# Optimization experiments

Measured on AMD Instinct MI355X. Metric: run time of the kernel, lower is better.

Reference implementation:

```python
import jax, jax.numpy as jnp
import numpy as np

INPUT_DIM, HIDDEN_DIM, OUTPUT_DIM = 64, 512, 64
BATCH, SEQ = 256, 512


def setup_inputs() -> dict:
    key = jax.random.key(0)
    ks = jax.random.split(key, 7)
    s_x = 1.0 / np.sqrt(INPUT_DIM)
    s_h = 1.0 / np.sqrt(HIDDEN_DIM)
    return {
        "x": jax.random.normal(ks[0], (BATCH, SEQ, INPUT_DIM), dtype=jnp.float32),
        "Wx": jax.random.uniform(ks[1], (HIDDEN_DIM, INPUT_DIM), minval=-s_x, maxval=s_x, dtype=jnp.float32),
        "bx": jax.random.uniform(ks[2], (HIDDEN_DIM,), minval=-s_x, maxval=s_x, dtype=jnp.float32),
        "Wh": jax.random.uniform(ks[3], (HIDDEN_DIM, HIDDEN_DIM), minval=-s_h, maxval=s_h, dtype=jnp.float32),
        "bh": jax.random.uniform(ks[4], (HIDDEN_DIM,), minval=-s_h, maxval=s_h, dtype=jnp.float32),
        "Wy": jax.random.uniform(ks[5], (OUTPUT_DIM, HIDDEN_DIM), minval=-s_h, maxval=s_h, dtype=jnp.float32),
        "by": jax.random.uniform(ks[6], (OUTPUT_DIM,), minval=-s_h, maxval=s_h, dtype=jnp.float32),
    }


def reference(x, Wx, bx, Wh, bh, Wy, by):
    # x: [B, T, I]. Precompute the input projection for all steps (one big GEMM),
    # then scan the sequential recurrence h_t = tanh(xproj_t + h_{t-1} @ Wh^T + bh).
    B = x.shape[0]
    xproj = jnp.einsum('bti,hi->bth', x, Wx) + bx  # [B, T, H]
    h0 = jnp.zeros((B, Wh.shape[0]), dtype=x.dtype)

    def step(h, xp_t):
        h = jnp.tanh(xp_t + h @ Wh.T + bh)
        return h, None

    hT, _ = jax.lax.scan(step, h0, jnp.swapaxes(xproj, 0, 1))  # scan over T
    y = hT @ Wy.T + by  # [B, O]
    return y
```

## Files before the change

### kernel.cpp

```cpp
#include <hip/hip_runtime.h>
#include <hip/hip_fp16.h>
#include <cstdint>
#include <cstddef>


constexpr int BATCH = 256;
constexpr int SEQ   = 512;
constexpr int IN    = 64;
constexpr int HID   = 512;
constexpr int OUT   = 64;
constexpr int T     = 512;
constexpr int DTOT  = HID + IN;
constexpr int DSL   = DTOT / 8;
constexpr int NL    = 19;
constexpr int KL0   = 53;

typedef _Float16 half2v __attribute__((ext_vector_type(2)));

__device__ __forceinline__ float fdot2(uint32_t w, uint32_t h, float acc) {
    return __builtin_amdgcn_fdot2(__builtin_bit_cast(half2v, w),
                                  __builtin_bit_cast(half2v, h), acc, false);
}
__device__ __forceinline__ uint32_t packh2(float lo, float hi) {
    return (uint32_t)__half_as_ushort(__float2half(lo)) |
           ((uint32_t)__half_as_ushort(__float2half(hi)) << 16);
}
template <int CTRL>
__device__ __forceinline__ float dpp_add(float v) {
    int i = __builtin_bit_cast(int, v);
    int p = __builtin_amdgcn_update_dpp(i, i, CTRL, 0xF, 0xF, false);
    return v + __builtin_bit_cast(float, p);
}

__global__ __launch_bounds__(256, 1)
void prep_w(const float* __restrict__ Wh, const float* __restrict__ Wx,
            uint4* __restrict__ Wpk) {
    const int idx = blockIdx.x * 256 + threadIdx.x;
    const int k = idx >> 9, t = idx & (T - 1);
    const int p = k >> 3, r = k & 7;
    const int g = t >> 3, s = t & 7;
    const int o = 8 * g + r;
    const int d0 = DSL * s + 8 * p;
    const float* src = (d0 < HID) ? (Wh + (size_t)o * HID + d0)
                                  : (Wx + (size_t)o * IN + (d0 - HID));
    uint4 d;
    d.x = packh2(src[0], src[1]);
    d.y = packh2(src[2], src[3]);
    d.z = packh2(src[4], src[5]);
    d.w = packh2(src[6], src[7]);
    Wpk[idx] = d;
}

#define MV(f, Z) { \
    Z = fdot2(w##f.x, hv.x, Z); Z = fdot2(w##f.y, hv.y, Z); \
    Z = fdot2(w##f.z, hv.z, Z); Z = fdot2(w##f.w, hv.w, Z); }
#define ML(i, Z) { const uint4 wv = wl[t * NL + (i)]; \
    Z = fdot2(wv.x, hv.x, Z); Z = fdot2(wv.y, hv.y, Z); \
    Z = fdot2(wv.z, hv.z, Z); Z = fdot2(wv.w, hv.w, Z); }

__global__ __launch_bounds__(T, 2)
__attribute__((amdgpu_waves_per_eu(2, 2)))
void rnn_main(const float* __restrict__ x,  const float* __restrict__ bx,
              const float* __restrict__ bh, const float* __restrict__ Wy,
              const float* __restrict__ by, const uint4* __restrict__ Wpk,
              float* __restrict__ y) {
    __shared__ uint4 wl[T * NL];
    __shared__ __align__(16) __half hb2[2][DTOT];

    const int b = blockIdx.x, t = threadIdx.x;
    const int s = t & 7;

    {
        uint32_t agk;
        asm volatile("v_accvgpr_write_b32 a127, 0\n\t"
                     "s_nop 1\n\t"
                     "v_accvgpr_read_b32 %0, a127" : "=v"(agk));
        if (agk == 0xDEADBEEFu) hb2[0][0] = __float2half(0.0f);
    }

    #pragma unroll
    for (int i = 0; i < NL; ++i)
        wl[t * NL + i] = Wpk[(size_t)(KL0 + i) * T + t];

#define DECL_WV(f) const uint4 w##f = Wpk[(size_t)(f) * T + t];
    DECL_WV(0)  DECL_WV(1)  DECL_WV(2)  DECL_WV(3)  DECL_WV(4)  DECL_WV(5)
    DECL_WV(6)  DECL_WV(7)  DECL_WV(8)  DECL_WV(9)  DECL_WV(10) DECL_WV(11)
    DECL_WV(12) DECL_WV(13) DECL_WV(14) DECL_WV(15) DECL_WV(16) DECL_WV(17)
    DECL_WV(18) DECL_WV(19) DECL_WV(20) DECL_WV(21) DECL_WV(22) DECL_WV(23)
    DECL_WV(24) DECL_WV(25) DECL_WV(26) DECL_WV(27) DECL_WV(28) DECL_WV(29)
    DECL_WV(30) DECL_WV(31) DECL_WV(32) DECL_WV(33) DECL_WV(34) DECL_WV(35)
    DECL_WV(36) DECL_WV(37) DECL_WV(38) DECL_WV(39) DECL_WV(40) DECL_WV(41)
    DECL_WV(42) DECL_WV(43) DECL_WV(44) DECL_WV(45) DECL_WV(46) DECL_WV(47)
    DECL_WV(48) DECL_WV(49) DECL_WV(50) DECL_WV(51) DECL_WV(52)
#undef DECL_WV

    const float bs = bx[t] + bh[t];
    const float* xb = x + (size_t)b * SEQ * IN;

    hb2[0][t] = __float2half(0.0f);
    if (t < IN) hb2[0][HID + t] = __float2half(xb[t]);
    float xv = (t < IN) ? xb[IN + t] : 0.0f;
    __syncthreads();

    #pragma unroll 1
    for (int tt = 0; tt < SEQ; ++tt) {
        const int c = tt & 1;
        const uint4* hb = (const uint4*)(&hb2[c][0] + DSL * s);
        float z0 = 0.f, z1 = 0.f, z2 = 0.f, z3 = 0.f;
        float z4 = 0.f, z5 = 0.f, z6 = 0.f, z7 = 0.f;

        { const uint4 hv = hb[0];
          MV(0,z0) MV(1,z1) MV(2,z2) MV(3,z3) MV(4,z4) MV(5,z5) MV(6,z6) MV(7,z7) }
        { const uint4 hv = hb[1];
          MV(8,z0) MV(9,z1) MV(10,z2) MV(11,z3) MV(12,z4) MV(13,z5) MV(14,z6) MV(15,z7) }
        { const uint4 hv = hb[2];
          MV(16,z0) MV(17,z1) MV(18,z2) MV(19,z3) MV(20,z4) MV(21,z5) MV(22,z6) MV(23,z7) }
        { const uint4 hv = hb[3];
          MV(24,z0) MV(25,z1) MV(26,z2) MV(27,z3) MV(28,z4) MV(29,z5) MV(30,z6) MV(31,z7) }
        { const uint4 hv = hb[4];
          MV(32,z0) MV(33,z1) MV(34,z2) MV(35,z3) MV(36,z4) MV(37,z5) MV(38,z6) MV(39,z7) }
        { const uint4 hv = hb[5];
          MV(40,z0) MV(41,z1) MV(42,z2) MV(43,z3) MV(44,z4) MV(45,z5) MV(46,z6) MV(47,z7) }
        { const uint4 hv = hb[6];
          MV(48,z0) MV(49,z1) MV(50,z2) MV(51,z3) MV(52,z4) ML(0,z5) ML(1,z6) ML(2,z7) }
        { const uint4 hv = hb[7];
          ML(3,z0) ML(4,z1) ML(5,z2) ML(6,z3) ML(7,z4) ML(8,z5) ML(9,z6) ML(10,z7) }
        { const uint4 hv = hb[8];
          ML(11,z0) ML(12,z1) ML(13,z2) ML(14,z3) ML(15,z4) ML(16,z5) ML(17,z6) ML(18,z7) }

        z0 = dpp_add<0xB1>(z0); z0 = dpp_add<0x4E>(z0); z0 = dpp_add<0x141>(z0);
        z1 = dpp_add<0xB1>(z1); z1 = dpp_add<0x4E>(z1); z1 = dpp_add<0x141>(z1);
        z2 = dpp_add<0xB1>(z2); z2 = dpp_add<0x4E>(z2); z2 = dpp_add<0x141>(z2);
        z3 = dpp_add<0xB1>(z3); z3 = dpp_add<0x4E>(z3); z3 = dpp_add<0x141>(z3);
        z4 = dpp_add<0xB1>(z4); z4 = dpp_add<0x4E>(z4); z4 = dpp_add<0x141>(z4);
        z5 = dpp_add<0xB1>(z5); z5 = dpp_add<0x4E>(z5); z5 = dpp_add<0x141>(z5);
        z6 = dpp_add<0xB1>(z6); z6 = dpp_add<0x4E>(z6); z6 = dpp_add<0x141>(z6);
        z7 = dpp_add<0xB1>(z7); z7 = dpp_add<0x4E>(z7); z7 = dpp_add<0x141>(z7);

        const float za = (s & 1) ? z1 : z0;
        const float zb = (s & 1) ? z3 : z2;
        const float zc = (s & 1) ? z5 : z4;
        const float zd = (s & 1) ? z7 : z6;
        const float ze = (s & 2) ? zb : za;
        const float zf = (s & 2) ? zd : zc;
        const float zz = (s & 4) ? zf : ze;
        const float hh = 1.f - 2.f * __builtin_amdgcn_rcpf(__expf(2.f * (zz + bs)) + 1.f);
        hb2[c ^ 1][t] = __float2half(hh);

        if (t < IN) {
            hb2[c ^ 1][HID + t] = __float2half(xv);
            if (tt + 2 < SEQ) xv = xb[(size_t)(tt + 2) * IN + t];
        }
        __syncthreads();
    }

    if (t < OUT) {
        float acc = by[t];
        const float* wy = Wy + (size_t)t * HID;
        #pragma unroll 8
        for (int j = 0; j < HID; ++j)
            acc = fmaf(wy[j], __half2float(hb2[0][j]), acc);
        y[(size_t)b * OUT + t] = acc;
    }
}

extern "C" void kernel_launch(void* const* d_in, const int* in_sizes, int n_in,
                              void* d_out, int out_size, void* d_ws, size_t ws_size,
                              hipStream_t stream) {
    const float* x  = (const float*)d_in[0];
    const float* Wx = (const float*)d_in[1];
    const float* bx = (const float*)d_in[2];
    const float* Wh = (const float*)d_in[3];
    const float* bh = (const float*)d_in[4];
    const float* Wy = (const float*)d_in[5];
    const float* by = (const float*)d_in[6];
    float* y = (float*)d_out;

    uint4* Wpk = (uint4*)d_ws;

    hipLaunchKernelGGL(prep_w, dim3(72 * T / 256), dim3(256), 0, stream,
                       Wh, Wx, Wpk);
    hipLaunchKernelGGL(rnn_main, dim3(BATCH), dim3(T), 0, stream,
                       x, bx, bh, Wy, by, Wpk, y);
}
```

Before: 879.2 us.

## Precompute input projection in separate GEMM kernel and shrink recurrent matvec

Adds a prep_xp kernel that computes x@Wx^T+bx for every batch and step into an fp16 workspace buffer. The recurrent kernel then only does the 512x512 hidden matvec (64 packed weight slices instead of 72) and adds the prefetched projection per step. This removes the x columns from the serial loop and reduces LDS-resident weights, at the cost of writing and reading a 128 MB fp16 intermediate and an extra launch. Falls back to the old path if the workspace is too small.

```diff
diff --git a/kernel.cpp b/kernel.cpp
--- a/kernel.cpp
+++ b/kernel.cpp
@@ -10,10 +10,6 @@
 constexpr int HID   = 512;
 constexpr int OUT   = 64;
 constexpr int T     = 512;
-constexpr int DTOT  = HID + IN;
-constexpr int DSL   = DTOT / 8;
-constexpr int NL    = 19;
-constexpr int KL0   = 53;
 
 typedef _Float16 half2v __attribute__((ext_vector_type(2)));
 
@@ -32,17 +28,14 @@
     return v + __builtin_bit_cast(float, p);
 }
 
+
 __global__ __launch_bounds__(256, 1)
-void prep_w(const float* __restrict__ Wh, const float* __restrict__ Wx,
-            uint4* __restrict__ Wpk) {
+void prep_w64(const float* __restrict__ Wh, uint4* __restrict__ Wpk) {
     const int idx = blockIdx.x * 256 + threadIdx.x;
     const int k = idx >> 9, t = idx & (T - 1);
     const int p = k >> 3, r = k & 7;
     const int g = t >> 3, s = t & 7;
-    const int o = 8 * g + r;
-    const int d0 = DSL * s + 8 * p;
-    const float* src = (d0 < HID) ? (Wh + (size_t)o * HID + d0)
-                                  : (Wx + (size_t)o * IN + (d0 - HID));
+    const float* src = Wh + (size_t)(8 * g + r) * HID + (64 * s + 8 * p);
     uint4 d;
     d.x = packh2(src[0], src[1]);
     d.y = packh2(src[2], src[3]);
@@ -51,21 +44,56 @@
     Wpk[idx] = d;
 }
 
+__global__ __launch_bounds__(256, 1)
+void prep_xp(const float* __restrict__ x, const float* __restrict__ Wx,
+             const float* __restrict__ bx, __half* __restrict__ XPh) {
+    __shared__ uint32_t xs2[16][32];
+    const int tid = threadIdx.x;
+    const size_t R0 = (size_t)blockIdx.x * 16;
+
+    for (int e = tid; e < 16 * 32; e += 256) {
+        const int r = e >> 5, j = e & 31;
+        const float2 v = *(const float2*)(x + (R0 + r) * IN + 2 * j);
+        xs2[r][j] = packh2(v.x, v.y);
+    }
+    const int c0 = 2 * tid, c1 = c0 + 1;
+    uint32_t wa[32], wb[32];
+    #pragma unroll
+    for (int q = 0; q < 16; ++q) {
+        const float4 va = *(const float4*)(Wx + (size_t)c0 * IN + 4 * q);
+        wa[2 * q] = packh2(va.x, va.y); wa[2 * q + 1] = packh2(va.z, va.w);
+        const float4 vb = *(const float4*)(Wx + (size_t)c1 * IN + 4 * q);
+        wb[2 * q] = packh2(vb.x, vb.y); wb[2 * q + 1] = packh2(vb.z, vb.w);
+    }
+    const float b0 = bx[c0], b1 = bx[c1];
+    __syncthreads();
+
+    for (int r = 0; r < 16; ++r) {
+        float a0 = b0, a1 = b1;
+        #pragma unroll
+        for (int j = 0; j < 32; ++j) {
+            const uint32_t hx = xs2[r][j];
+            a0 = fdot2(wa[j], hx, a0);
+            a1 = fdot2(wb[j], hx, a1);
+        }
+        ((uint32_t*)XPh)[((R0 + r) * HID + c0) >> 1] = packh2(a0, a1);
+    }
+}
+
 #define MV(f, Z) { \
     Z = fdot2(w##f.x, hv.x, Z); Z = fdot2(w##f.y, hv.y, Z); \
     Z = fdot2(w##f.z, hv.z, Z); Z = fdot2(w##f.w, hv.w, Z); }
-#define ML(i, Z) { const uint4 wv = wl[t * NL + (i)]; \
+#define ML(i, Z) { const uint4 wv = wl[(i) * T + t]; \
     Z = fdot2(wv.x, hv.x, Z); Z = fdot2(wv.y, hv.y, Z); \
     Z = fdot2(wv.z, hv.z, Z); Z = fdot2(wv.w, hv.w, Z); }
 
 __global__ __launch_bounds__(T, 2)
 __attribute__((amdgpu_waves_per_eu(2, 2)))
-void rnn_main(const float* __restrict__ x,  const float* __restrict__ bx,
-              const float* __restrict__ bh, const float* __restrict__ Wy,
-              const float* __restrict__ by, const uint4* __restrict__ Wpk,
-              float* __restrict__ y) {
-    __shared__ uint4 wl[T * NL];
-    __shared__ __align__(16) __half hb2[2][DTOT];
+void rnn_main64(const float* __restrict__ bh, const float* __restrict__ Wy,
+                const float* __restrict__ by, const uint4* __restrict__ Wpk,
+                const __half* __restrict__ XPh, float* __restrict__ y) {
+    __shared__ uint4 wl[11 * T];
+    __shared__ __align__(16) __half hb2[2][HID];
 
     const int b = blockIdx.x, t = threadIdx.x;
     const int s = t & 7;
@@ -79,8 +107,8 @@
     }
 
     #pragma unroll
-    for (int i = 0; i < NL; ++i)
-        wl[t * NL + i] = Wpk[(size_t)(KL0 + i) * T + t];
+    for (int i = 0; i < 11; ++i)
+        wl[i * T + t] = Wpk[(size_t)(53 + i) * T + t];
 
 #define DECL_WV(f) const uint4 w##f = Wpk[(size_t)(f) * T + t];
     DECL_WV(0)  DECL_WV(1)  DECL_WV(2)  DECL_WV(3)  DECL_WV(4)  DECL_WV(5)
@@ -94,18 +122,20 @@
     DECL_WV(48) DECL_WV(49) DECL_WV(50) DECL_WV(51) DECL_WV(52)
 #undef DECL_WV
 
-    const float bs = bx[t] + bh[t];
-    const float* xb = x + (size_t)b * SEQ * IN;
+    const float bs = bh[t];
+    const __half* XProw = XPh + ((size_t)b * SEQ) * HID + t;
 
     hb2[0][t] = __float2half(0.0f);
-    if (t < IN) hb2[0][HID + t] = __float2half(xb[t]);
-    float xv = (t < IN) ? xb[IN + t] : 0.0f;
+    float xpc = __half2float(XProw[0]);
     __syncthreads();
 
     #pragma unroll 1
     for (int tt = 0; tt < SEQ; ++tt) {
         const int c = tt & 1;
-        const uint4* hb = (const uint4*)(&hb2[c][0] + DSL * s);
+        float xpn = 0.0f;
+        if (tt + 1 < SEQ) xpn = __half2float(XProw[(size_t)(tt + 1) * HID]);
+
+        const uint4* hb = (const uint4*)(&hb2[c][0] + 64 * s);
         float z0 = 0.f, z1 = 0.f, z2 = 0.f, z3 = 0.f;
         float z4 = 0.f, z5 = 0.f, z6 = 0.f, z7 = 0.f;
 
@@ -125,8 +155,136 @@
           MV(48,z0) MV(49,z1) MV(50,z2) MV(51,z3) MV(52,z4) ML(0,z5) ML(1,z6) ML(2,z7) }
         { const uint4 hv = hb[7];
           ML(3,z0) ML(4,z1) ML(5,z2) ML(6,z3) ML(7,z4) ML(8,z5) ML(9,z6) ML(10,z7) }
+
+        z0 = dpp_add<0xB1>(z0); z0 = dpp_add<0x4E>(z0); z0 = dpp_add<0x141>(z0);
+        z1 = dpp_add<0xB1>(z1); z1 = dpp_add<0x4E>(z1); z1 = dpp_add<0x141>(z1);
+        z2 = dpp_add<0xB1>(z2); z2 = dpp_add<0x4E>(z2); z2 = dpp_add<0x141>(z2);
+        z3 = dpp_add<0xB1>(z3); z3 = dpp_add<0x4E>(z3); z3 = dpp_add<0x141>(z3);
+        z4 = dpp_add<0xB1>(z4); z4 = dpp_add<0x4E>(z4); z4 = dpp_add<0x141>(z4);
+        z5 = dpp_add<0xB1>(z5); z5 = dpp_add<0x4E>(z5); z5 = dpp_add<0x141>(z5);
+        z6 = dpp_add<0xB1>(z6); z6 = dpp_add<0x4E>(z6); z6 = dpp_add<0x141>(z6);
+        z7 = dpp_add<0xB1>(z7); z7 = dpp_add<0x4E>(z7); z7 = dpp_add<0x141>(z7);
+
+        const float za = (s & 1) ? z1 : z0;
+        const float zb = (s & 1) ? z3 : z2;
+        const float zc = (s & 1) ? z5 : z4;
+        const float zd = (s & 1) ? z7 : z6;
+        const float ze = (s & 2) ? zb : za;
+        const float zf = (s & 2) ? zd : zc;
+        const float zz = (s & 4) ? zf : ze;
+        const float hh = 1.f - 2.f * __builtin_amdgcn_rcpf(
+                             __expf(2.f * (zz + bs + xpc)) + 1.f);
+        hb2[c ^ 1][t] = __float2half(hh);
+        xpc = xpn;
+        __syncthreads();
+    }
+
+    if (t < OUT) {
+        float acc = by[t];
+        const float* wy = Wy + (size_t)t * HID;
+        #pragma unroll 8
+        for (int j = 0; j < HID; ++j)
+            acc = fmaf(wy[j], __half2float(hb2[0][j]), acc);
+        y[(size_t)b * OUT + t] = acc;
+    }
+}
+
+
+constexpr int DTOT  = HID + IN;
+constexpr int DSL72 = DTOT / 8;
+constexpr int NL72  = 19;
+constexpr int KL072 = 53;
+
+__global__ __launch_bounds__(256, 1)
+void prep_w72(const float* __restrict__ Wh, const float* __restrict__ Wx,
+              uint4* __restrict__ Wpk) {
+    const int idx = blockIdx.x * 256 + threadIdx.x;
+    const int k = idx >> 9, t = idx & (T - 1);
+    const int p = k >> 3, r = k & 7;
+    const int g = t >> 3, s = t & 7;
+    const int o = 8 * g + r;
+    const int d0 = DSL72 * s + 8 * p;
+    const float* src = (d0 < HID) ? (Wh + (size_t)o * HID + d0)
+                                  : (Wx + (size_t)o * IN + (d0 - HID));
+    uint4 d;
+    d.x = packh2(src[0], src[1]);
+    d.y = packh2(src[2], src[3]);
+    d.z = packh2(src[4], src[5]);
+    d.w = packh2(src[6], src[7]);
+    Wpk[idx] = d;
+}
+
+#define ML72(i, Z) { const uint4 wv = wl[t * NL72 + (i)]; \
+    Z = fdot2(wv.x, hv.x, Z); Z = fdot2(wv.y, hv.y, Z); \
+    Z = fdot2(wv.z, hv.z, Z); Z = fdot2(wv.w, hv.w, Z); }
+
+__global__ __launch_bounds__(T, 2)
+__attribute__((amdgpu_waves_per_eu(2, 2)))
+void rnn_main72(const float* __restrict__ x,  const float* __restrict__ bx,
+                const float* __restrict__ bh, const float* __restrict__ Wy,
+                const float* __restrict__ by, const uint4* __restrict__ Wpk,
+                float* __restrict__ y) {
+    __shared__ uint4 wl[T * NL72];
+    __shared__ __align__(16) __half hb2[2][DTOT];
+
+    const int b = blockIdx.x, t = threadIdx.x;
+    const int s = t & 7;
+    {
+        uint32_t agk;
+        asm volatile("v_accvgpr_write_b32 a127, 0\n\t"
+                     "s_nop 1\n\t"
+                     "v_accvgpr_read_b32 %0, a127" : "=v"(agk));
+        if (agk == 0xDEADBEEFu) hb2[0][0] = __float2half(0.0f);
+    }
+    #pragma unroll
+    for (int i = 0; i < NL72; ++i)
+        wl[t * NL72 + i] = Wpk[(size_t)(KL072 + i) * T + t];
+
+#define DECL_WV(f) const uint4 w##f = Wpk[(size_t)(f) * T + t];
+    DECL_WV(0)  DECL_WV(1)  DECL_WV(2)  DECL_WV(3)  DECL_WV(4)  DECL_WV(5)
+    DECL_WV(6)  DECL_WV(7)  DECL_WV(8)  DECL_WV(9)  DECL_WV(10) DECL_WV(11)
+    DECL_WV(12) DECL_WV(13) DECL_WV(14) DECL_WV(15) DECL_WV(16) DECL_WV(17)
+    DECL_WV(18) DECL_WV(19) DECL_WV(20) DECL_WV(21) DECL_WV(22) DECL_WV(23)
+    DECL_WV(24) DECL_WV(25) DECL_WV(26) DECL_WV(27) DECL_WV(28) DECL_WV(29)
+    DECL_WV(30) DECL_WV(31) DECL_WV(32) DECL_WV(33) DECL_WV(34) DECL_WV(35)
+    DECL_WV(36) DECL_WV(37) DECL_WV(38) DECL_WV(39) DECL_WV(40) DECL_WV(41)
+    DECL_WV(42) DECL_WV(43) DECL_WV(44) DECL_WV(45) DECL_WV(46) DECL_WV(47)
+    DECL_WV(48) DECL_WV(49) DECL_WV(50) DECL_WV(51) DECL_WV(52)
+#undef DECL_WV
+
+    const float bs = bx[t] + bh[t];
+    const float* xb = x + (size_t)b * SEQ * IN;
+
+    hb2[0][t] = __float2half(0.0f);
+    if (t < IN) hb2[0][HID + t] = __float2half(xb[t]);
+    float xv = (t < IN) ? xb[IN + t] : 0.0f;
+    __syncthreads();
+
+    #pragma unroll 1
+    for (int tt = 0; tt < SEQ; ++tt) {
+        const int c = tt & 1;
+        const uint4* hb = (const uint4*)(&hb2[c][0] + DSL72 * s);
+        float z0 = 0.f, z1 = 0.f, z2 = 0.f, z3 = 0.f;
+        float z4 = 0.f, z5 = 0.f, z6 = 0.f, z7 = 0.f;
+
+        { const uint4 hv = hb[0];
+          MV(0,z0) MV(1,z1) MV(2,z2) MV(3,z3) MV(4,z4) MV(5,z5) MV(6,z6) MV(7,z7) }
+        { const uint4 hv = hb[1];
+          MV(8,z0) MV(9,z1) MV(10,z2) MV(11,z3) MV(12,z4) MV(13,z5) MV(14,z6) MV(15,z7) }
+        { const uint4 hv = hb[2];
+          MV(16,z0) MV(17,z1) MV(18,z2) MV(19,z3) MV(20,z4) MV(21,z5) MV(22,z6) MV(23,z7) }
+        { const uint4 hv = hb[3];
+          MV(24,z0) MV(25,z1) MV(26,z2) MV(27,z3) MV(28,z4) MV(29,z5) MV(30,z6) MV(31,z7) }
+        { const uint4 hv = hb[4];
+          MV(32,z0) MV(33,z1) MV(34,z2) MV(35,z3) MV(36,z4) MV(37,z5) MV(38,z6) MV(39,z7) }
+        { const uint4 hv = hb[5];
+          MV(40,z0) MV(41,z1) MV(42,z2) MV(43,z3) MV(44,z4) MV(45,z5) MV(46,z6) MV(47,z7) }
+        { const uint4 hv = hb[6];
+          MV(48,z0) MV(49,z1) MV(50,z2) MV(51,z3) MV(52,z4) ML72(0,z5) ML72(1,z6) ML72(2,z7) }
+        { const uint4 hv = hb[7];
+          ML72(3,z0) ML72(4,z1) ML72(5,z2) ML72(6,z3) ML72(7,z4) ML72(8,z5) ML72(9,z6) ML72(10,z7) }
         { const uint4 hv = hb[8];
-          ML(11,z0) ML(12,z1) ML(13,z2) ML(14,z3) ML(15,z4) ML(16,z5) ML(17,z6) ML(18,z7) }
+          ML72(11,z0) ML72(12,z1) ML72(13,z2) ML72(14,z3) ML72(15,z4) ML72(16,z5) ML72(17,z6) ML72(18,z7) }
 
         z0 = dpp_add<0xB1>(z0); z0 = dpp_add<0x4E>(z0); z0 = dpp_add<0x141>(z0);
         z1 = dpp_add<0xB1>(z1); z1 = dpp_add<0x4E>(z1); z1 = dpp_add<0x141>(z1);
@@ -176,10 +334,22 @@
     const float* by = (const float*)d_in[6];
     float* y = (float*)d_out;
 
-    uint4* Wpk = (uint4*)d_ws;
-
-    hipLaunchKernelGGL(prep_w, dim3(72 * T / 256), dim3(256), 0, stream,
-                       Wh, Wx, Wpk);
-    hipLaunchKernelGGL(rnn_main, dim3(BATCH), dim3(T), 0, stream,
-                       x, bx, bh, Wy, by, Wpk, y);
-}
+    const size_t wpk_bytes = (size_t)72 * T * 16;
+    const size_t xp_bytes  = (size_t)BATCH * SEQ * HID * 2;
+    if (ws_size >= wpk_bytes + xp_bytes) {
+        uint4*  Wpk = (uint4*)d_ws;
+        __half* XPh = (__half*)((char*)d_ws + wpk_bytes);
+        hipLaunchKernelGGL(prep_w64, dim3(64 * T / 256), dim3(256), 0, stream,
+                           Wh, Wpk);
+        hipLaunchKernelGGL(prep_xp, dim3(BATCH * SEQ / 16), dim3(256), 0, stream,
+                           x, Wx, bx, XPh);
+        hipLaunchKernelGGL(rnn_main64, dim3(BATCH), dim3(T), 0, stream,
+                           bh, Wy, by, Wpk, XPh, y);
+    } else {
+        uint4* Wpk = (uint4*)d_ws;
+        hipLaunchKernelGGL(prep_w72, dim3(72 * T / 256), dim3(256), 0, stream,
+                           Wh, Wx, Wpk);
+        hipLaunchKernelGGL(rnn_main72, dim3(BATCH), dim3(T), 0, stream,
+                           x, bx, bh, Wy, by, Wpk, y);
+    }
+}
```

Measured after the change: 1.047 ms. 1.19x slower.

## Halve threads per block, compute two hidden units per thread

Applied to the files above, without the earlier changes.

Each block now uses 256 threads instead of 512, and each thread produces two hidden outputs with 16 accumulators. The packed weight layout is regenerated for 16 rows per group, with 113 fragments kept in registers and 31 in LDS. Occupancy drops to one wave per EU so the larger register file can hold more weights. The goal is fewer threads doing less redundant h-vector LDS reads and synchronization per step, at the cost of more serial work per thread and a longer dependency chain.

```diff
diff --git a/kernel.cpp b/kernel.cpp
--- a/kernel.cpp
+++ b/kernel.cpp
@@ -9,11 +9,12 @@
 constexpr int IN    = 64;
 constexpr int HID   = 512;
 constexpr int OUT   = 64;
-constexpr int T     = 512;
+constexpr int T     = 256;
 constexpr int DTOT  = HID + IN;
 constexpr int DSL   = DTOT / 8;
-constexpr int NL    = 19;
-constexpr int KL0   = 53;
+constexpr int NF    = 144;
+constexpr int NSSA  = 113;
+constexpr int NL    = 31;
 
 typedef _Float16 half2v __attribute__((ext_vector_type(2)));
 
@@ -36,10 +37,10 @@
 void prep_w(const float* __restrict__ Wh, const float* __restrict__ Wx,
             uint4* __restrict__ Wpk) {
     const int idx = blockIdx.x * 256 + threadIdx.x;
-    const int k = idx >> 9, t = idx & (T - 1);
-    const int p = k >> 3, r = k & 7;
+    const int k = idx >> 8, t = idx & (T - 1);
+    const int p = k >> 4, r = k & 15;
     const int g = t >> 3, s = t & 7;
-    const int o = 8 * g + r;
+    const int o = 16 * g + r;
     const int d0 = DSL * s + 8 * p;
     const float* src = (d0 < HID) ? (Wh + (size_t)o * HID + d0)
                                   : (Wx + (size_t)o * IN + (d0 - HID));
@@ -51,6 +52,20 @@
     Wpk[idx] = d;
 }
 
+#define RG_LIST(M) \
+  M(0)   M(1)   M(2)   M(3)   M(4)   M(5)   M(6)   M(7)   M(8)   M(9)  \
+  M(10)  M(11)  M(12)  M(13)  M(14)  M(15)  M(16)  M(17)  M(18)  M(19) \
+  M(20)  M(21)  M(22)  M(23)  M(24)  M(25)  M(26)  M(27)  M(28)  M(29) \
+  M(30)  M(31)  M(32)  M(33)  M(34)  M(35)  M(36)  M(37)  M(38)  M(39) \
+  M(40)  M(41)  M(42)  M(43)  M(44)  M(45)  M(46)  M(47)  M(48)  M(49) \
+  M(50)  M(51)  M(52)  M(53)  M(54)  M(55)  M(56)  M(57)  M(58)  M(59) \
+  M(60)  M(61)  M(62)  M(63)  M(64)  M(65)  M(66)  M(67)  M(68)  M(69) \
+  M(70)  M(71)  M(72)  M(73)  M(74)  M(75)  M(76)  M(77)  M(78)  M(79) \
+  M(80)  M(81)  M(82)  M(83)  M(84)  M(85)  M(86)  M(87)  M(88)  M(89) \
+  M(90)  M(91)  M(92)  M(93)  M(94)  M(95)  M(96)  M(97)  M(98)  M(99) \
+  M(100) M(101) M(102) M(103) M(104) M(105) M(106) M(107) M(108) M(109) \
+  M(110) M(111) M(112)
+
 #define MV(f, Z) { \
     Z = fdot2(w##f.x, hv.x, Z); Z = fdot2(w##f.y, hv.y, Z); \
     Z = fdot2(w##f.z, hv.z, Z); Z = fdot2(w##f.w, hv.w, Z); }
@@ -58,8 +73,8 @@
     Z = fdot2(wv.x, hv.x, Z); Z = fdot2(wv.y, hv.y, Z); \
     Z = fdot2(wv.z, hv.z, Z); Z = fdot2(wv.w, hv.w, Z); }
 
-__global__ __launch_bounds__(T, 2)
-__attribute__((amdgpu_waves_per_eu(2, 2)))
+__global__ __launch_bounds__(T, 1)
+__attribute__((amdgpu_waves_per_eu(1, 1)))
 void rnn_main(const float* __restrict__ x,  const float* __restrict__ bx,
               const float* __restrict__ bh, const float* __restrict__ Wy,
               const float* __restrict__ by, const uint4* __restrict__ Wpk,
@@ -72,32 +87,25 @@
 
     {
         uint32_t agk;
-        asm volatile("v_accvgpr_write_b32 a127, 0\n\t"
+        asm volatile("v_accvgpr_write_b32 a255, 0\n\t"
                      "s_nop 1\n\t"
-                     "v_accvgpr_read_b32 %0, a127" : "=v"(agk));
+                     "v_accvgpr_read_b32 %0, a255" : "=v"(agk));
         if (agk == 0xDEADBEEFu) hb2[0][0] = __float2half(0.0f);
     }
 
     #pragma unroll
     for (int i = 0; i < NL; ++i)
-        wl[t * NL + i] = Wpk[(size_t)(KL0 + i) * T + t];
+        wl[t * NL + i] = Wpk[(size_t)(NSSA + i) * T + t];
 
 #define DECL_WV(f) const uint4 w##f = Wpk[(size_t)(f) * T + t];
-    DECL_WV(0)  DECL_WV(1)  DECL_WV(2)  DECL_WV(3)  DECL_WV(4)  DECL_WV(5)
-    DECL_WV(6)  DECL_WV(7)  DECL_WV(8)  DECL_WV(9)  DECL_WV(10) DECL_WV(11)
-    DECL_WV(12) DECL_WV(13) DECL_WV(14) DECL_WV(15) DECL_WV(16) DECL_WV(17)
-    DECL_WV(18) DECL_WV(19) DECL_WV(20) DECL_WV(21) DECL_WV(22) DECL_WV(23)
-    DECL_WV(24) DECL_WV(25) DECL_WV(26) DECL_WV(27) DECL_WV(28) DECL_WV(29)
-    DECL_WV(30) DECL_WV(31) DECL_WV(32) DECL_WV(33) DECL_WV(34) DECL_WV(35)
-    DECL_WV(36) DECL_WV(37) DECL_WV(38) DECL_WV(39) DECL_WV(40) DECL_WV(41)
-    DECL_WV(42) DECL_WV(43) DECL_WV(44) DECL_WV(45) DECL_WV(46) DECL_WV(47)
-    DECL_WV(48) DECL_WV(49) DECL_WV(50) DECL_WV(51) DECL_WV(52)
+    RG_LIST(DECL_WV)
 #undef DECL_WV
 
-    const float bs = bx[t] + bh[t];
+    const float bs0 = bx[2 * t]     + bh[2 * t];
+    const float bs1 = bx[2 * t + 1] + bh[2 * t + 1];
     const float* xb = x + (size_t)b * SEQ * IN;
 
-    hb2[0][t] = __float2half(0.0f);
+    ((uint32_t*)hb2[0])[t] = 0u;
     if (t < IN) hb2[0][HID + t] = __float2half(xb[t]);
     float xv = (t < IN) ? xb[IN + t] : 0.0f;
     __syncthreads();
@@ -106,46 +114,83 @@
     for (int tt = 0; tt < SEQ; ++tt) {
         const int c = tt & 1;
         const uint4* hb = (const uint4*)(&hb2[c][0] + DSL * s);
-        float z0 = 0.f, z1 = 0.f, z2 = 0.f, z3 = 0.f;
-        float z4 = 0.f, z5 = 0.f, z6 = 0.f, z7 = 0.f;
+        float z0  = 0.f, z1  = 0.f, z2  = 0.f, z3  = 0.f;
+        float z4  = 0.f, z5  = 0.f, z6  = 0.f, z7  = 0.f;
+        float z8  = 0.f, z9  = 0.f, z10 = 0.f, z11 = 0.f;
+        float z12 = 0.f, z13 = 0.f, z14 = 0.f, z15 = 0.f;
 
         { const uint4 hv = hb[0];
-          MV(0,z0) MV(1,z1) MV(2,z2) MV(3,z3) MV(4,z4) MV(5,z5) MV(6,z6) MV(7,z7) }
+          MV(0,z0)   MV(1,z1)   MV(2,z2)   MV(3,z3)   MV(4,z4)   MV(5,z5)
+          MV(6,z6)   MV(7,z7)   MV(8,z8)   MV(9,z9)   MV(10,z10) MV(11,z11)
+          MV(12,z12) MV(13,z13) MV(14,z14) MV(15,z15) }
         { const uint4 hv = hb[1];
-          MV(8,z0) MV(9,z1) MV(10,z2) MV(11,z3) MV(12,z4) MV(13,z5) MV(14,z6) MV(15,z7) }
+          MV(16,z0)  MV(17,z1)  MV(18,z2)  MV(19,z3)  MV(20,z4)  MV(21,z5)
+          MV(22,z6)  MV(23,z7)  MV(24,z8)  MV(25,z9)  MV(26,z10) MV(27,z11)
+          MV(28,z12) MV(29,z13) MV(30,z14) MV(31,z15) }
         { const uint4 hv = hb[2];
-          MV(16,z0) MV(17,z1) MV(18,z2) MV(19,z3) MV(20,z4) MV(21,z5) MV(22,z6) MV(23,z7) }
+          MV(32,z0)  MV(33,z1)  MV(34,z2)  MV(35,z3)  MV(36,z4)  MV(37,z5)
+          MV(38,z6)  MV(39,z7)  MV(40,z8)  MV(41,z9)  MV(42,z10) MV(43,z11)
+          MV(44,z12) MV(45,z13) MV(46,z14) MV(47,z15) }
         { const uint4 hv = hb[3];
-          MV(24,z0) MV(25,z1) MV(26,z2) MV(27,z3) MV(28,z4) MV(29,z5) MV(30,z6) MV(31,z7) }
+          MV(48,z0)  MV(49,z1)  MV(50,z2)  MV(51,z3)  MV(52,z4)  MV(53,z5)
+          MV(54,z6)  MV(55,z7)  MV(56,z8)  MV(57,z9)  MV(58,z10) MV(59,z11)
+          MV(60,z12) MV(61,z13) MV(62,z14) MV(63,z15) }
         { const uint4 hv = hb[4];
-          MV(32,z0) MV(33,z1) MV(34,z2) MV(35,z3) MV(36,z4) MV(37,z5) MV(38,z6) MV(39,z7) }
+          MV(64,z0)  MV(65,z1)  MV(66,z2)  MV(67,z3)  MV(68,z4)  MV(69,z5)
+          MV(70,z6)  MV(71,z7)  MV(72,z8)  MV(73,z9)  MV(74,z10) MV(75,z11)
+          MV(76,z12) MV(77,z13) MV(78,z14) MV(79,z15) }
         { const uint4 hv = hb[5];
-          MV(40,z0) MV(41,z1) MV(42,z2) MV(43,z3) MV(44,z4) MV(45,z5) MV(46,z6) MV(47,z7) }
+          MV(80,z0)  MV(81,z1)  MV(82,z2)  MV(83,z3)  MV(84,z4)  MV(85,z5)
+          MV(86,z6)  MV(87,z7)  MV(88,z8)  MV(89,z9)  MV(90,z10) MV(91,z11)
+          MV(92,z12) MV(93,z13) MV(94,z14) MV(95,z15) }
         { const uint4 hv = hb[6];
-          MV(48,z0) MV(49,z1) MV(50,z2) MV(51,z3) MV(52,z4) ML(0,z5) ML(1,z6) ML(2,z7) }
+          MV(96,z0)  MV(97,z1)  MV(98,z2)  MV(99,z3)  MV(100,z4) MV(101,z5)
+          MV(102,z6) MV(103,z7) MV(104,z8) MV(105,z9) MV(106,z10) MV(107,z11)
+          MV(108,z12) MV(109,z13) MV(110,z14) MV(111,z15) }
         { const uint4 hv = hb[7];
-          ML(3,z0) ML(4,z1) ML(5,z2) ML(6,z3) ML(7,z4) ML(8,z5) ML(9,z6) ML(10,z7) }
+          MV(112,z0) ML(0,z1)   ML(1,z2)   ML(2,z3)   ML(3,z4)   ML(4,z5)
+          ML(5,z6)   ML(6,z7)   ML(7,z8)   ML(8,z9)   ML(9,z10)  ML(10,z11)
+          ML(11,z12) ML(12,z13) ML(13,z14) ML(14,z15) }
         { const uint4 hv = hb[8];
-          ML(11,z0) ML(12,z1) ML(13,z2) ML(14,z3) ML(15,z4) ML(16,z5) ML(17,z6) ML(18,z7) }
-
-        z0 = dpp_add<0xB1>(z0); z0 = dpp_add<0x4E>(z0); z0 = dpp_add<0x141>(z0);
-        z1 = dpp_add<0xB1>(z1); z1 = dpp_add<0x4E>(z1); z1 = dpp_add<0x141>(z1);
-        z2 = dpp_add<0xB1>(z2); z2 = dpp_add<0x4E>(z2); z2 = dpp_add<0x141>(z2);
-        z3 = dpp_add<0xB1>(z3); z3 = dpp_add<0x4E>(z3); z3 = dpp_add<0x141>(z3);
-        z4 = dpp_add<0xB1>(z4); z4 = dpp_add<0x4E>(z4); z4 = dpp_add<0x141>(z4);
-        z5 = dpp_add<0xB1>(z5); z5 = dpp_add<0x4E>(z5); z5 = dpp_add<0x141>(z5);
-        z6 = dpp_add<0xB1>(z6); z6 = dpp_add<0x4E>(z6); z6 = dpp_add<0x141>(z6);
-        z7 = dpp_add<0xB1>(z7); z7 = dpp_add<0x4E>(z7); z7 = dpp_add<0x141>(z7);
-
-        const float za = (s & 1) ? z1 : z0;
-        const float zb = (s & 1) ? z3 : z2;
-        const float zc = (s & 1) ? z5 : z4;
-        const float zd = (s & 1) ? z7 : z6;
-        const float ze = (s & 2) ? zb : za;
-        const float zf = (s & 2) ? zd : zc;
-        const float zz = (s & 4) ? zf : ze;
-        const float hh = 1.f - 2.f * __builtin_amdgcn_rcpf(__expf(2.f * (zz + bs)) + 1.f);
-        hb2[c ^ 1][t] = __float2half(hh);
+          ML(15,z0)  ML(16,z1)  ML(17,z2)  ML(18,z3)  ML(19,z4)  ML(20,z5)
+          ML(21,z6)  ML(22,z7)  ML(23,z8)  ML(24,z9)  ML(25,z10) ML(26,z11)
+          ML(27,z12) ML(28,z13) ML(29,z14) ML(30,z15) }
+
+        z0  = dpp_add<0xB1>(z0);  z0  = dpp_add<0x4E>(z0);  z0  = dpp_add<0x141>(z0);
+        z1  = dpp_add<0xB1>(z1);  z1  = dpp_add<0x4E>(z1);  z1  = dpp_add<0x141>(z1);
+        z2  = dpp_add<0xB1>(z2);  z2  = dpp_add<0x4E>(z2);  z2  = dpp_add<0x141>(z2);
+        z3  = dpp_add<0xB1>(z3);  z3  = dpp_add<0x4E>(z3);  z3  = dpp_add<0x141>(z3);
+        z4  = dpp_add<0xB1>(z4);  z4  = dpp_add<0x4E>(z4);  z4  = dpp_add<0x141>(z4);
+        z5  = dpp_add<0xB1>(z5);  z5  = dpp_add<0x4E>(z5);  z5  = dpp_add<0x141>(z5);
+        z6  = dpp_add<0xB1>(z6);  z6  = dpp_add<0x4E>(z6);  z6  = dpp_add<0x141>(z6);
+        z7  = dpp_add<0xB1>(z7);  z7  = dpp_add<0x4E>(z7);  z7  = dpp_add<0x141>(z7);
+        z8  = dpp_add<0xB1>(z8);  z8  = dpp_add<0x4E>(z8);  z8  = dpp_add<0x141>(z8);
+        z9  = dpp_add<0xB1>(z9);  z9  = dpp_add<0x4E>(z9);  z9  = dpp_add<0x141>(z9);
+        z10 = dpp_add<0xB1>(z10); z10 = dpp_add<0x4E>(z10); z10 = dpp_add<0x141>(z10);
+        z11 = dpp_add<0xB1>(z11); z11 = dpp_add<0x4E>(z11); z11 = dpp_add<0x141>(z11);
+        z12 = dpp_add<0xB1>(z12); z12 = dpp_add<0x4E>(z12); z12 = dpp_add<0x141>(z12);
+        z13 = dpp_add<0xB1>(z13); z13 = dpp_add<0x4E>(z13); z13 = dpp_add<0x141>(z13);
+        z14 = dpp_add<0xB1>(z14); z14 = dpp_add<0x4E>(z14); z14 = dpp_add<0x141>(z14);
+        z15 = dpp_add<0xB1>(z15); z15 = dpp_add<0x4E>(z15); z15 = dpp_add<0x141>(z15);
+
+        const float ea = (s & 1) ? z2  : z0;
+        const float eb = (s & 1) ? z6  : z4;
+        const float ec = (s & 1) ? z10 : z8;
+        const float ed = (s & 1) ? z14 : z12;
+        const float ee = (s & 2) ? eb  : ea;
+        const float ef = (s & 2) ? ed  : ec;
+        const float zE = (s & 4) ? ef  : ee;
+        const float oa = (s & 1) ? z3  : z1;
+        const float ob = (s & 1) ? z7  : z5;
+        const float oc = (s & 1) ? z11 : z9;
+        const float od = (s & 1) ? z15 : z13;
+        const float oe = (s & 2) ? ob  : oa;
+        const float of_ = (s & 2) ? od : oc;
+        const float zO = (s & 4) ? of_ : oe;
+
+        const float h0 = 1.f - 2.f * __builtin_amdgcn_rcpf(__expf(2.f * (zE + bs0)) + 1.f);
+        const float h1 = 1.f - 2.f * __builtin_amdgcn_rcpf(__expf(2.f * (zO + bs1)) + 1.f);
+        ((uint32_t*)hb2[c ^ 1])[t] = packh2(h0, h1);
 
         if (t < IN) {
             hb2[c ^ 1][HID + t] = __float2half(xv);
@@ -178,7 +223,7 @@
 
     uint4* Wpk = (uint4*)d_ws;
 
-    hipLaunchKernelGGL(prep_w, dim3(72 * T / 256), dim3(256), 0, stream,
+    hipLaunchKernelGGL(prep_w, dim3(NF * T / 256), dim3(256), 0, stream,
                        Wh, Wx, Wpk);
     hipLaunchKernelGGL(rnn_main, dim3(BATCH), dim3(T), 0, stream,
                        x, bx, bh, Wy, by, Wpk, y);
```

Result: slower. 1.578 ms (+79.5%).
